# Kernel optimization log

Measured on AMD Instinct MI355X. Metric: run time of the kernel, lower is better.

The kernel has to match this reference:

```python
import jax, jax.numpy as jnp
import numpy as np

EPS_SHIFT = 1e-8   # additive epsilon used by the original code
EPS_NORM = 1e-12   # torch.nn.functional.normalize default eps


def setup_inputs() -> dict:
    key = jax.random.key(0)
    inputs = jax.random.normal(key, (1024, 2048, 3, 3), dtype=jnp.float32)
    return {"inputs": inputs}


def reference(inputs):
    # inputs: (B, num_res, 3, 3) -> flat atom chain (B, N, 3), N = 3*num_res
    B, R = inputs.shape[0], inputs.shape[1]
    x = inputs.reshape(B, R * 3, 3)

    # sliding 4-atom windows, vectorized over all N-3 dihedrals
    a = x[:, :-3, :]
    b = x[:, 1:-2, :]
    c = x[:, 2:-1, :]
    d = x[:, 3:, :]

    bc_raw = b - c + EPS_SHIFT
    bc = bc_raw / jnp.clip(
        jnp.linalg.norm(bc_raw, axis=-1, keepdims=True), EPS_NORM)

    n1 = jnp.cross(a - b, bc)          # (B, N-3, 3)
    n2 = jnp.cross(bc, c - d)          # (B, N-3, 3)
    xc = jnp.sum(n1 * n2, axis=-1)     # (B, N-3)
    yc = jnp.sum(jnp.cross(n1, bc) * n2, axis=-1)
    dih = jnp.arctan2(yc, xc + EPS_SHIFT)

    # original concatenates all sin values then all cos values along last dim
    angles = jnp.concatenate([jnp.sin(dih), jnp.cos(dih)], axis=-1)  # (B, 2*(N-3))
    first_three = x[:, :3, :]                                        # (B, 3, 3)
    return (angles, first_three)
```

## Files before the change

kernel.cpp:

```cpp
#include <hip/hip_runtime.h>

#define ROWS 1024
#define PTS 6144
#define NDIH (PTS - 3)
#define ROWF (PTS * 3)
#define CHUNK 1024
#define DPT 4
#define THREADS 256
#define NCHUNK 6
#define ANG_PER_ROW (2 * NDIH)
#define SFLOATS ((CHUNK + 3) * 3 + 3)
#define EPS_SHIFT 1e-8f

__global__ __launch_bounds__(THREADS) void dih_kernel(const float* __restrict__ in,
                                                      float* __restrict__ out) {
    __shared__ float s[SFLOATS];
    const int b     = blockIdx.x / NCHUNK;
    const int chunk = blockIdx.x % NCHUNK;
    const int i0    = chunk * CHUNK;
    const int t     = threadIdx.x;

    const float* row = in + (size_t)b * ROWF;
    const int base = i0 * 3;
    const int n4 = min(SFLOATS / 4, (ROWF - base) / 4);
    const float4* g4 = (const float4*)(row + base);
    float4* s4 = (float4*)s;
    for (int k = t; k < n4; k += THREADS) s4[k] = g4[k];
    __syncthreads();

    if (chunk == 0 && t < 9)
        out[(size_t)ROWS * ANG_PER_ROW + (size_t)b * 9 + t] = s[t];

    float w[21];
    {
        const float4* ls4 = (const float4*)(s + 12 * t);
        float4 v0 = ls4[0], v1 = ls4[1], v2 = ls4[2], v3 = ls4[3], v4 = ls4[4];
        w[0]=v0.x;  w[1]=v0.y;  w[2]=v0.z;  w[3]=v0.w;
        w[4]=v1.x;  w[5]=v1.y;  w[6]=v1.z;  w[7]=v1.w;
        w[8]=v2.x;  w[9]=v2.y;  w[10]=v2.z; w[11]=v2.w;
        w[12]=v3.x; w[13]=v3.y; w[14]=v3.z; w[15]=v3.w;
        w[16]=v4.x; w[17]=v4.y; w[18]=v4.z; w[19]=v4.w;
        w[20]=s[12 * t + 20];
    }

    float ex[6], ey[6], ez[6];
    #pragma unroll
    for (int j = 0; j < 6; ++j) {
        ex[j] = w[3*j + 0] - w[3*j + 3];
        ey[j] = w[3*j + 1] - w[3*j + 4];
        ez[j] = w[3*j + 2] - w[3*j + 5];
    }

    float sv[DPT], cv[DPT];
    #pragma unroll
    for (int k = 0; k < DPT; ++k) {
        const float brx = ex[k+1] + EPS_SHIFT;
        const float bry = ey[k+1] + EPS_SHIFT;
        const float brz = ez[k+1] + EPS_SHIFT;
        const float nrm2 = brx*brx + bry*bry + brz*brz;
        const float inv = rsqrtf(fmaxf(nrm2, 1e-24f));
        const float ux = brx * inv, uy = bry * inv, uz = brz * inv;

        const float n1x = ey[k]*uz - ez[k]*uy;
        const float n1y = ez[k]*ux - ex[k]*uz;
        const float n1z = ex[k]*uy - ey[k]*ux;
        const float n2x = uy*ez[k+2] - uz*ey[k+2];
        const float n2y = uz*ex[k+2] - ux*ez[k+2];
        const float n2z = ux*ey[k+2] - uy*ex[k+2];

        const float xc = n1x*n2x + n1y*n2y + n1z*n2z;
        const float mx = n1y*uz - n1z*uy;
        const float my = n1z*ux - n1x*uz;
        const float mz = n1x*uy - n1y*ux;
        const float yc = mx*n2x + my*n2y + mz*n2z;

        const float xz = xc + EPS_SHIFT;
        const float r2 = yc*yc + xz*xz;
        const float rinv = rsqrtf(fmaxf(r2, 1e-30f));
        sv[k] = (r2 > 0.0f) ? yc * rinv : 0.0f;
        cv[k] = (r2 > 0.0f) ? xz * rinv : 1.0f;
    }

    __syncthreads();
    ((float4*)s)[t]           = make_float4(sv[0], sv[1], sv[2], sv[3]);
    ((float4*)(s + CHUNK))[t] = make_float4(cv[0], cv[1], cv[2], cv[3]);
    __syncthreads();

    const size_t obase = (size_t)b * ANG_PER_ROW;
    const int valid = min(CHUNK, NDIH - i0);
    float* so = out + obase + i0;
    float* co = out + obase + NDIH + i0;
    #pragma unroll
    for (int k = 0; k < 4; ++k) {
        const int j = k * THREADS + t;
        if (j < valid) {
            so[j] = s[j];
            co[j] = s[CHUNK + j];
        }
    }
}

extern "C" void kernel_launch(void* const* d_in, const int* in_sizes, int n_in,
                              void* d_out, int out_size, void* d_ws, size_t ws_size,
                              hipStream_t stream) {
    const float* in = (const float*)d_in[0];
    float* out = (float*)d_out;
    dih_kernel<<<dim3(ROWS * NCHUNK), dim3(THREADS), 0, stream>>>(in, out);
}
```

Measured before the change: 119.7 us.

## Load input via per-wave global_load_lds and store angles directly from registers

Replaces the cooperative block-wide float4 copy into shared memory with per-wave direct global-to-LDS loads. Each wave fetches only the slice it later reads, including a small halo, so the block-wide barrier becomes a wave-local vmcnt wait. The output path drops the shared-memory staging and its two barriers. Sin values are written as float2 pairs and cos values as scalars straight from registers. The trade-off is less contiguous per-lane stores and overlapping halo writes between waves, which are benign because the values are identical.

```diff
diff --git a/kernel.cpp b/kernel.cpp
--- a/kernel.cpp
+++ b/kernel.cpp
@@ -4,6 +4,7 @@
 #define PTS 6144
 #define NDIH (PTS - 3)
 #define ROWF (PTS * 3)
+#define ROWF4 (ROWF / 4)
 #define CHUNK 1024
 #define DPT 4
 #define THREADS 256
@@ -12,6 +13,7 @@
 #define SFLOATS ((CHUNK + 3) * 3 + 3)
 #define EPS_SHIFT 1e-8f
 
+
 __global__ __launch_bounds__(THREADS) void dih_kernel(const float* __restrict__ in,
                                                       float* __restrict__ out) {
     __shared__ float s[SFLOATS];
@@ -19,14 +21,24 @@
     const int chunk = blockIdx.x % NCHUNK;
     const int i0    = chunk * CHUNK;
     const int t     = threadIdx.x;
+    const int wid   = t >> 6;
+    const int lane  = t & 63;
 
-    const float* row = in + (size_t)b * ROWF;
-    const int base = i0 * 3;
-    const int n4 = min(SFLOATS / 4, (ROWF - base) / 4);
-    const float4* g4 = (const float4*)(row + base);
-    float4* s4 = (float4*)s;
-    for (int k = t; k < n4; k += THREADS) s4[k] = g4[k];
-    __syncthreads();
+    const float4* g4  = (const float4*)(in + (size_t)b * ROWF);
+    const int cbase   = chunk * (CHUNK * 3 / 4);
+    #pragma unroll
+    for (int p = 0; p < 4; ++p) {
+        const int rel = p * 64 + lane;
+        const int f4i = 192 * wid + rel;
+        if (rel < 195 && (cbase + f4i) < ROWF4) {
+            __builtin_amdgcn_global_load_lds(
+                (const __attribute__((address_space(1))) void*)(g4 + cbase + f4i),
+                (__attribute__((address_space(3))) void*)(s + (192 * wid + p * 64) * 4),
+                16, 0, 0);
+        }
+    }
+    asm volatile("s_waitcnt vmcnt(0)" ::: "memory");
+    __builtin_amdgcn_sched_barrier(0);
 
     if (chunk == 0 && t < 9)
         out[(size_t)ROWS * ANG_PER_ROW + (size_t)b * 9 + t] = s[t];
@@ -81,22 +93,19 @@
         cv[k] = (r2 > 0.0f) ? xz * rinv : 1.0f;
     }
 
-    __syncthreads();
-    ((float4*)s)[t]           = make_float4(sv[0], sv[1], sv[2], sv[3]);
-    ((float4*)(s + CHUNK))[t] = make_float4(cv[0], cv[1], cv[2], cv[3]);
-    __syncthreads();
-
     const size_t obase = (size_t)b * ANG_PER_ROW;
-    const int valid = min(CHUNK, NDIH - i0);
     float* so = out + obase + i0;
     float* co = out + obase + NDIH + i0;
-    #pragma unroll
-    for (int k = 0; k < 4; ++k) {
-        const int j = k * THREADS + t;
-        if (j < valid) {
-            so[j] = s[j];
-            co[j] = s[CHUNK + j];
-        }
+    const int j0    = 4 * t;
+    const int valid = NDIH - i0;
+    if (j0 + 3 < valid) {
+        *(float2*)(so + j0)     = make_float2(sv[0], sv[1]);
+        *(float2*)(so + j0 + 2) = make_float2(sv[2], sv[3]);
+        co[j0+0] = cv[0]; co[j0+1] = cv[1]; co[j0+2] = cv[2]; co[j0+3] = cv[3];
+    } else {
+        #pragma unroll
+        for (int k = 0; k < 4; ++k)
+            if (j0 + k < valid) { so[j0+k] = sv[k]; co[j0+k] = cv[k]; }
     }
 }
 
```

Measured after the change: 118.8 us. About the same (-0.7%).
